# Kernel tuning notes

Measured on AMD Instinct MI355X. Metric: run time of the kernel, lower is better.

## Reference

```python
import jax, jax.numpy as jnp
import numpy as np
from jax.scipy.ndimage import map_coordinates

N = 512      # image H=W (x0.shape[2])
A = 30       # number of projection angles (sparse-view CT)
D = 729      # det_count (hardcoded in source)
L = 3        # LayerNo
B = 2        # batch
P = 2048     # FFT padding: next pow2 >= 2*D


def _ramp_filter(size):
    # standard Ram-Lak filter built in spatial domain (skimage/torch-radon style)
    n = np.concatenate((np.arange(1, size // 2 + 1, 2), np.arange(size // 2 - 1, 0, -2)))
    f = np.zeros(size)
    f[0] = 0.25
    f[1::2] = -1.0 / (np.pi * n) ** 2
    return jnp.asarray(2.0 * np.real(np.fft.fft(f))[: size // 2 + 1], dtype=jnp.float32)


def setup_inputs() -> dict:
    key = jax.random.key(0)
    ks = jax.random.split(key, 8)
    x0 = jax.random.normal(ks[0], (B, 1, N, N), jnp.float32)
    sinogram = jax.random.normal(ks[1], (B, 1, A, D), jnp.float32)
    theta = jnp.linspace(0.0, np.pi, A, endpoint=False).astype(jnp.float32)
    theta_label = theta
    # denoiser params, stacked over L unrolled layers
    w1 = jax.random.normal(ks[2], (L, 32, 1, 3, 3), jnp.float32) * 0.1
    b1 = jnp.zeros((L, 32), jnp.float32)
    w2 = jax.random.normal(ks[3], (L, 32, 32, 3, 3), jnp.float32) * 0.05
    b2 = jnp.zeros((L, 32), jnp.float32)
    w3 = jax.random.normal(ks[4], (L, 32, 32, 3, 3), jnp.float32) * 0.05
    b3 = jnp.zeros((L, 32), jnp.float32)
    w4 = jax.random.normal(ks[5], (L, 1, 32, 3, 3), jnp.float32) * 0.05
    steps = jnp.ones((L,), jnp.float32)  # step_n params (requires_grad=False)
    return {"cond": 1, "x0": x0, "sinogram": sinogram, "theta": theta,
            "theta_label": theta_label, "w1": w1, "b1": b1, "w2": w2, "b2": b2,
            "w3": w3, "b3": b3, "w4": w4, "steps": steps}


def _conv(x, w, b=None):
    y = jax.lax.conv_general_dilated(x, w, (1, 1), 'SAME',
                                     dimension_numbers=('NCHW', 'OIHW', 'NCHW'))
    return y if b is None else y + b[None, :, None, None]


def _denoiser(x, w1, b1, w2, b2, w3, b3, w4):
    h = jax.nn.relu(_conv(x, w1, b1))
    h = jax.nn.relu(_conv(h, w2, b2))
    h = jax.nn.relu(_conv(h, w3, b3))
    return _conv(h, w4)


def _geometry(theta):
    # parallel-beam ray sampling grid: rows/cols [A, D, T] with T=D samples (dt=1)
    c = (N - 1) / 2.0
    s = jnp.arange(D, dtype=jnp.float32) - (D - 1) / 2.0  # detector coords
    t = s                                                  # along-ray samples
    cs, sn = jnp.cos(theta), jnp.sin(theta)
    x = s[None, :, None] * cs[:, None, None] - t[None, None, :] * sn[:, None, None]
    y = s[None, :, None] * sn[:, None, None] + t[None, None, :] * cs[:, None, None]
    return y + c, x + c  # rows, cols


def _radon_fwd(imgs, rows, cols):
    # imgs [B,N,N] -> sinogram [B,A,D] via bilinear line-integral sampling
    sample = lambda im: map_coordinates(im, [rows, cols], order=1, mode='constant', cval=0.0)
    return jax.vmap(sample)(imgs).sum(-1)


def _filter_sino(sino, filt):
    F = jnp.fft.rfft(sino, n=P, axis=-1)
    g = jnp.fft.irfft(F * filt, n=P, axis=-1)[..., :D]
    return g * (jnp.pi / (2.0 * A))  # FBP normalization


def _backproj(sino, theta):
    # sino [B,A,D] -> image [B,N,N], linear interp along detector axis
    c = (N - 1) / 2.0
    xs = jnp.arange(N, dtype=jnp.float32) - c
    cs, sn = jnp.cos(theta), jnp.sin(theta)
    sgrid = cs[:, None, None] * xs[None, None, :] + sn[:, None, None] * xs[None, :, None]  # [A,N,N]
    idx = sgrid + (D - 1) / 2.0
    lo = jnp.floor(idx).astype(jnp.int32)
    w = idx - lo
    lo_ok = (lo >= 0) & (lo < D)
    hi_ok = (lo + 1 >= 0) & (lo + 1 < D)
    lo_c = jnp.clip(lo, 0, D - 1)
    hi_c = jnp.clip(lo + 1, 0, D - 1)
    a = jnp.arange(A)[:, None, None]
    v = sino[:, a, lo_c] * jnp.where(lo_ok, 1.0 - w, 0.0) + \
        sino[:, a, hi_c] * jnp.where(hi_ok, w, 0.0)       # [B,A,N,N]
    return v.sum(axis=1)


def reference(cond, x0, sinogram, theta, theta_label, w1, b1, w2, b2, w3, b3, w4, steps):
    rows, cols = _geometry(theta)
    filt = _ramp_filter(P)
    X = x0[:, 0]           # [B,N,N]
    sino = sinogram[:, 0]  # [B,A,D]
    for n in range(L):
        sino_pred = _radon_fwd(X, rows, cols)
        filtered = _filter_sino(sino_pred, filt)
        outputs = _backproj(sino - filtered, theta)
        z = X + steps[n] * outputs
        noise = _denoiser(X[:, None], w1[n], b1[n], w2[n], b2[n], w3[n], b3[n], w4[n])[:, 0]
        filtered_noise = _filter_sino(_radon_fwd(noise, rows, cols), filt)
        outputs_noise = _backproj(filtered_noise, theta)
        X = z + noise - steps[n] * outputs_noise
    Xo = X[:, None]
    return (Xo, Xo, Xo)
```

## Files before the change

kernel.cpp:

```cpp
#include <hip/hip_runtime.h>
#include <hip/hip_bf16.h>

typedef __hip_bfloat16 bf16;
typedef __attribute__((ext_vector_type(8))) short short8;
typedef __attribute__((ext_vector_type(4))) short s4v;
typedef __attribute__((ext_vector_type(4))) float float4v;

#define NN 512
#define NA 30
#define ND 729
#define NB 2
#define NL 3
#define BNN (NB*NN*NN)
#define BAD (NB*NA*ND)

#define PW 520
#define PH 516
#define PIMG (PH*PW)
#define POFF (2*PW + 2)

#define O_CS  0
#define O_SN  32
#define O_ICS 64
#define O_ISN 96
#define O_XP  128
#define O_YP  (O_XP + 2*PIMG)
#define O_SP  (O_YP + 2*PIMG)
#define O_Q   (O_SP + BAD)
#define O_WR  (O_Q + BAD)
#define O_H   (((O_WR + 34560) + 15) & ~15)
#define H_FLOATS (NB * 32 * NN * NN / 2)

#define WR2_OFF 0
#define WR3_OFF 27648
#define WR4_OFF 55296

__device__ __forceinline__ float2 ld2u(const float* p)
{
    float2 r;
    __builtin_memcpy(&r, p, 8);
    return r;
}

__global__ void k_prep(const float* __restrict__ theta,
                       const float* __restrict__ w2, const float* __restrict__ w3,
                       const float* __restrict__ w4, const float* __restrict__ x0,
                       float* __restrict__ ws, bf16* __restrict__ wr)
{
    int idx = blockIdx.x * 256 + threadIdx.x;
    if (idx < NA) {
        float t = theta[idx];
        float cs = cosf(t), sn = sinf(t);
        ws[O_CS + idx] = cs;
        ws[O_SN + idx] = sn;
        ws[O_ICS + idx] = 1.0f / cs;
        ws[O_ISN + idx] = -1.0f / sn;
    }
    if (idx < 2 * 27648) {
        const float* w = (idx < 27648) ? w2 : w3;
        int base = (idx < 27648) ? WR2_OFF : WR3_OFF;
        int r = idx % 27648;
        int n = r / 9216; int r2 = r % 9216;
        int tap = r2 / 1024; int r3 = r2 % 1024;
        int co = r3 / 32, ci = r3 % 32;
        wr[base + r] = __float2bfloat16(w[n * 9216 + (co * 32 + ci) * 9 + tap]);
    } else if (idx < 2 * 27648 + 3 * 4608) {
        int r = idx - 2 * 27648;
        int n = r / 4608; int r2 = r % 4608;
        int tap = r2 / 512; int r3 = r2 % 512;
        int co = r3 / 32, ci = r3 % 32;
        float v = (co == 0) ? w4[n * 288 + ci * 9 + tap] : 0.f;
        wr[WR4_OFF + r] = __float2bfloat16(v);
    }
    if (idx < 2 * PIMG) {
        int b = idx / PIMG, p = idx % PIMG;
        int y = p / PW, x = p % PW;
        bool interior = (y >= 2 && y < 2 + NN && x >= 2 && x < 2 + NN);
        float v = interior ? x0[b * NN * NN + (y - 2) * NN + (x - 2)] : 0.f;
        ws[O_XP + idx] = v;
        if (!interior) ws[O_YP + idx] = 0.f;
    }
}

__device__ __forceinline__ void isect2(float A, float inv, float lo, float hi,
                                       float& tlo, float& thi)
{
    float a = (lo - A) * inv, b = (hi - A) * inv;
    tlo = fmaxf(tlo, fminf(a, b));
    thi = fminf(thi, fmaxf(a, b));
}

__global__ __launch_bounds__(256) void k_radon(const float* __restrict__ img,
    const float* __restrict__ ws, float* __restrict__ out)
{
    int b = blockIdx.z, a = blockIdx.y;
    int wave = threadIdx.x >> 6;
    int lane = threadIdx.x & 63;
    int s = blockIdx.x * 4 + wave;
    if (s >= ND) return;
    float cs = ws[O_CS + a], sn = ws[O_SN + a];
    float ics = ws[O_ICS + a], isn = ws[O_ISN + a];
    float s_c = (float)s - 364.0f;
    float A_r = 255.5f + s_c * sn;
    float A_c = 255.5f + s_c * cs;

    float tlo = -1e9f, thi = 1e9f;
    isect2(A_r, ics, -1.0f, 512.0f, tlo, thi);
    isect2(A_c, isn, -1.0f, 512.0f, tlo, thi);
    float t0f = fmaxf(tlo + 364.0f, 0.0f);
    float t1f = fminf(thi + 364.0f, 728.0f);

    float acc = 0.f;
    if (t0f <= t1f) {
        int tb = (int)ceilf(t0f);
        int te = (int)floorf(t1f);
        const float* im = img + b * PIMG;
#pragma unroll 2
        for (int t = tb + lane; t <= te; t += 64) {
            float tc = (float)t - 364.0f;
            float r = fmaf(tc, cs, A_r);
            float c = fmaf(-tc, sn, A_c);
            float rf = floorf(r), cf = floorf(c);
            float dr = r - rf, dc = c - cf;
            int idx = (int)rf * PW + (int)cf;
            float2 tp = ld2u(im + idx);
            float2 bt = ld2u(im + idx + PW);
            float top = fmaf(dc, tp.y - tp.x, tp.x);
            float bot = fmaf(dc, bt.y - bt.x, bt.x);
            acc = fmaf(dr, bot - top, acc + top);
        }
    }
    acc += __shfl_down(acc, 32, 64);
    acc += __shfl_down(acc, 16, 64);
    acc += __shfl_down(acc, 8, 64);
    acc += __shfl_down(acc, 4, 64);
    acc += __shfl_down(acc, 2, 64);
    acc += __shfl_down(acc, 1, 64);
    if (lane == 0) out[(b * NA + a) * ND + s] = acc;
}

__global__ void k_filter(const float* __restrict__ sp, const float* __restrict__ sino,
                         float* __restrict__ q)
{
    __shared__ float row[ND];
    __shared__ float taps[364];
    int ba = blockIdx.y;
    const float* src = sp + ba * ND;
    for (int i = threadIdx.x; i < ND; i += 256) row[i] = src[i];
    const float PI2 = 9.86960440108936f;
    for (int i = threadIdx.x; i < 364; i += 256) {
        float m = (float)(2 * i + 1);
        taps[i] = -2.0f / (PI2 * m * m);
    }
    __syncthreads();
    const float scale = 0.0523598775598299f;
    int d = blockIdx.x * 256 + threadIdx.x;
    if (d < ND) {
        float g0 = 0.5f * row[d], g1 = 0.f;
#pragma unroll 4
        for (int j = 0; j < 364; j += 2) {
            int m0 = 2 * j + 1, m1 = 2 * j + 3;
            float l0 = (d - m0 >= 0) ? row[d - m0] : 0.f;
            float r0 = (d + m0 < ND) ? row[d + m0] : 0.f;
            g0 = fmaf(taps[j], l0 + r0, g0);
            float l1 = (d - m1 >= 0) ? row[d - m1] : 0.f;
            float r1 = (d + m1 < ND) ? row[d + m1] : 0.f;
            g1 = fmaf(taps[j + 1], l1 + r1, g1);
        }
        q[ba * ND + d] = sino[ba * ND + d] - scale * (g0 + g1);
    }
}

__global__ __launch_bounds__(256) void k_backproj_update(const float* __restrict__ q,
    const float* __restrict__ src1, const float* __restrict__ ws,
    const float* __restrict__ steps, int n, float* __restrict__ out,
    float* __restrict__ outcopy)
{
    __shared__ float qt[NA][28];
    __shared__ int dmin_s[NA];
    int b = blockIdx.z;
    int x0 = blockIdx.x * 16, y0 = blockIdx.y * 16;
    int tid = threadIdx.x;
    int lx = tid & 15, ly = tid >> 4;
    const float* qb = q + b * NA * ND;

    for (int idx = tid; idx < NA * 26; idx += 256) {
        int a = idx / 26, j = idx % 26;
        float cs = ws[O_CS + a], sn = ws[O_SN + a];
        float f00 = fmaf(cs, (float)x0 - 255.5f, fmaf(sn, (float)y0 - 255.5f, 364.0f));
        float fmn = f00 + fminf(cs * 15.f, 0.f) + fminf(sn * 15.f, 0.f);
        int dm = (int)floorf(fmn);
        if (j == 0) dmin_s[a] = dm;
        int d = dm + j;
        qt[a][j] = (d >= 0 && d < ND) ? qb[a * ND + d] : 0.f;
    }
    __syncthreads();

    float xc = (float)(x0 + lx) - 255.5f, yc = (float)(y0 + ly) - 255.5f;
    float acc = 0.f;
#pragma unroll
    for (int a = 0; a < NA; a++) {
        float cs = ws[O_CS + a], sn = ws[O_SN + a];
        float f = fmaf(cs, xc, fmaf(sn, yc, 364.0f));
        float lf = floorf(f);
        float w = f - lf;
        int j = (int)lf - dmin_s[a];
        float v0 = qt[a][j], v1 = qt[a][j + 1];
        acc = fmaf(v0, 1.0f - w, fmaf(v1, w, acc));
    }
    int pidx = b * PIMG + (y0 + ly) * PW + (x0 + lx);
    float v = fmaf(steps[n], acc, src1[pidx]);
    out[pidx] = v;
    if (outcopy) {
        int fidx = b * NN * NN + (y0 + ly) * NN + (x0 + lx);
        outcopy[fidx] = v;
        outcopy[fidx + BNN] = v;
        outcopy[fidx + 2 * BNN] = v;
    }
}

__global__ __launch_bounds__(256) void k_conv12(const float* __restrict__ XPb,
    const float* __restrict__ W1, const float* __restrict__ B1,
    const bf16* __restrict__ Wr2, const float* __restrict__ B2,
    bf16* __restrict__ outb)
{
    __shared__ bf16 h1t[34][18][32];
    int b = blockIdx.z;
    int x0 = blockIdx.x * 16;
    int Y0 = blockIdx.y * 32;
    const float* in = XPb + b * PIMG;

    for (int p = threadIdx.x; p < 34 * 18; p += 256) {
        int yy = p / 18, xx = p % 18;
        int gy = Y0 + yy - 1, gx = x0 + xx - 1;
        if (gy < 0 || gy >= NN || gx < 0 || gx >= NN) {
#pragma unroll
            for (int g = 0; g < 4; g++)
                *(short8*)(&h1t[yy][xx][g * 8]) = short8{};
        } else {
            float v[9];
#pragma unroll
            for (int dy = 0; dy < 3; dy++)
#pragma unroll
                for (int dx = 0; dx < 3; dx++)
                    v[dy * 3 + dx] = in[(gy + dy - 1) * PW + (gx + dx - 1)];
#pragma unroll
            for (int g = 0; g < 4; g++) {
                short8 pk;
#pragma unroll
                for (int j = 0; j < 8; j++) {
                    int co = g * 8 + j;
                    float a = B1[co];
                    const float* w = W1 + co * 9;
#pragma unroll
                    for (int k = 0; k < 9; k++) a = fmaf(v[k], w[k], a);
                    a = fmaxf(a, 0.f);
                    bf16 h = __float2bfloat16(a);
                    pk[j] = *reinterpret_cast<short*>(&h);
                }
                *(short8*)(&h1t[yy][xx][g * 8]) = pk;
            }
        }
    }
    __syncthreads();

    int lane = threadIdx.x & 63;
    int wave = threadIdx.x >> 6;
    int n16 = lane & 15, quad = lane >> 4;
    int y0w = Y0 + wave * 8;

    short8 wf[18];
#pragma unroll
    for (int tap = 0; tap < 9; tap++)
#pragma unroll
        for (int t = 0; t < 2; t++)
            wf[tap * 2 + t] = *(const short8*)(Wr2 + ((tap * 2 + t) * 16 + n16) * 32 + quad * 8);

    short8 win[3][3];
    auto loadrow = [&](int yy, short8* dst) {
        int ly = yy - (Y0 - 1);
#pragma unroll
        for (int dx = 0; dx < 3; dx++)
            dst[dx] = *(const short8*)(&h1t[ly][n16 + dx][quad * 8]);
    };
    loadrow(y0w - 1, win[0]);
    loadrow(y0w,     win[1]);

    float4v bias[2];
#pragma unroll
    for (int t = 0; t < 2; t++)
        bias[t] = *(const float4v*)(B2 + t * 16 + quad * 4);

    bf16* out = outb + (size_t)b * NN * NN * 32;
#pragma unroll
    for (int i = 0; i < 8; i++) {
        int y = y0w + i;
        loadrow(y + 1, win[(i + 2) % 3]);
        float4v acc[2];
#pragma unroll
        for (int t = 0; t < 2; t++) acc[t] = bias[t];
#pragma unroll
        for (int dy = 0; dy < 3; dy++) {
            short8* row = win[(i + dy) % 3];
#pragma unroll
            for (int dx = 0; dx < 3; dx++) {
                int tap = dy * 3 + dx;
#pragma unroll
                for (int t = 0; t < 2; t++)
                    acc[t] = __builtin_amdgcn_mfma_f32_16x16x32_bf16(wf[tap * 2 + t], row[dx], acc[t], 0, 0, 0);
            }
        }
        bf16* pp = out + ((size_t)y * NN + x0 + n16) * 32 + quad * 4;
#pragma unroll
        for (int t = 0; t < 2; t++) {
            s4v pk;
#pragma unroll
            for (int r = 0; r < 4; r++) {
                float v = fmaxf(acc[t][r], 0.f);
                bf16 h = __float2bfloat16(v);
                pk[r] = *reinterpret_cast<short*>(&h);
            }
            *(s4v*)(pp + t * 16) = pk;
        }
    }
}

#define SH 8
template<int NCO, bool RELU, bool HASB, bool OUTF32>
__global__ __launch_bounds__(256) void k_conv_stream(const bf16* __restrict__ inb,
    const bf16* __restrict__ Wr, const float* __restrict__ Bs,
    const float* __restrict__ addsrc, void* __restrict__ outv)
{
    int lane = threadIdx.x & 63;
    int wave = threadIdx.x >> 6;
    int n16 = lane & 15, quad = lane >> 4;
    int b = blockIdx.z;
    int x0 = blockIdx.x * 16;
    int y0 = (blockIdx.y * 4 + wave) * SH;
    const bf16* in = inb + (size_t)b * NN * NN * 32;

    short8 wf[9 * NCO];
#pragma unroll
    for (int tap = 0; tap < 9; tap++)
#pragma unroll
        for (int t = 0; t < NCO; t++)
            wf[tap * NCO + t] = *(const short8*)(Wr + ((tap * NCO + t) * 16 + n16) * 32 + quad * 8);

    bool vx[3];
#pragma unroll
    for (int dx = 0; dx < 3; dx++) {
        int xx = x0 + n16 + dx - 1;
        vx[dx] = (xx >= 0) && (xx < NN);
    }

    short8 win[3][3];
    auto loadrow = [&](int yy, short8* dst) {
        if (yy >= 0 && yy < NN) {
            const bf16* rowp = in + (size_t)yy * NN * 32;
#pragma unroll
            for (int dx = 0; dx < 3; dx++) {
                short8 v = {};
                if (vx[dx]) v = *(const short8*)(rowp + (x0 + n16 + dx - 1) * 32 + quad * 8);
                dst[dx] = v;
            }
        } else {
            dst[0] = short8{}; dst[1] = short8{}; dst[2] = short8{};
        }
    };
    loadrow(y0 - 1, win[0]);
    loadrow(y0,     win[1]);

    float4v bias[NCO];
#pragma unroll
    for (int t = 0; t < NCO; t++)
        bias[t] = HASB ? *(const float4v*)(Bs + t * 16 + quad * 4) : (float4v){0.f, 0.f, 0.f, 0.f};

#pragma unroll
    for (int i = 0; i < SH; i++) {
        int y = y0 + i;
        loadrow(y + 1, win[(i + 2) % 3]);
        float4v acc[NCO];
#pragma unroll
        for (int t = 0; t < NCO; t++) acc[t] = bias[t];
#pragma unroll
        for (int dy = 0; dy < 3; dy++) {
            short8* row = win[(i + dy) % 3];
#pragma unroll
            for (int dx = 0; dx < 3; dx++) {
                int tap = dy * 3 + dx;
#pragma unroll
                for (int t = 0; t < NCO; t++)
                    acc[t] = __builtin_amdgcn_mfma_f32_16x16x32_bf16(wf[tap * NCO + t], row[dx], acc[t], 0, 0, 0);
            }
        }
        if (OUTF32) {
            float* out = (float*)outv + b * PIMG;
            if (quad == 0) {
                int pi = y * PW + x0 + n16;
                out[pi] = addsrc[b * PIMG + pi] + acc[0][0];
            }
        } else {
            bf16* out = (bf16*)outv + (size_t)b * NN * NN * 32;
            bf16* pp = out + ((size_t)y * NN + x0 + n16) * 32 + quad * 4;
#pragma unroll
            for (int t = 0; t < NCO; t++) {
                s4v pk;
#pragma unroll
                for (int r = 0; r < 4; r++) {
                    float v = acc[t][r];
                    if (RELU) v = fmaxf(v, 0.f);
                    bf16 h = __float2bfloat16(v);
                    pk[r] = *reinterpret_cast<short*>(&h);
                }
                *(s4v*)(pp + t * 16) = pk;
            }
        }
    }
}

extern "C" void kernel_launch(void* const* d_in, const int* in_sizes, int n_in,
                              void* d_out, int out_size, void* d_ws, size_t ws_size,
                              hipStream_t stream)
{
    const float* x0    = (const float*)d_in[1];
    const float* sg    = (const float*)d_in[2];
    const float* theta = (const float*)d_in[3];
    const float* w1    = (const float*)d_in[5];
    const float* b1    = (const float*)d_in[6];
    const float* w2    = (const float*)d_in[7];
    const float* b2    = (const float*)d_in[8];
    const float* w3    = (const float*)d_in[9];
    const float* b3    = (const float*)d_in[10];
    const float* w4    = (const float*)d_in[11];
    const float* steps = (const float*)d_in[12];

    float* ws = (float*)d_ws;
    float* XP = ws + O_XP + POFF;
    float* YP = ws + O_YP + POFF;
    float* SP = ws + O_SP;
    float* Q  = ws + O_Q;
    bf16* wr  = (bf16*)(ws + O_WR);
    bf16* h1  = (bf16*)(ws + O_H);
    bf16* h2  = (bf16*)(ws + O_H + H_FLOATS);

    k_prep<<<(2 * PIMG + 255) / 256, 256, 0, stream>>>(theta, w2, w3, w4, x0, ws, wr);

    for (int n = 0; n < NL; n++) {
        k_conv12<<<dim3(32, 16, NB), 256, 0, stream>>>(
            XP, w1 + n * 288, b1 + n * 32, wr + WR2_OFF + n * 9216, b2 + n * 32, h2);
        k_conv_stream<2, true, true, false><<<dim3(32, 16, NB), 256, 0, stream>>>(
            h2, wr + WR3_OFF + n * 9216, b3 + n * 32, nullptr, h1);
        k_conv_stream<1, false, false, true><<<dim3(32, 16, NB), 256, 0, stream>>>(
            h1, wr + WR4_OFF + n * 4608, nullptr, XP, YP);

        k_radon<<<dim3((ND + 3) / 4, NA, NB), 256, 0, stream>>>(YP, ws, SP);
        k_filter<<<dim3(3, NB * NA), 256, 0, stream>>>(SP, sg, Q);
        k_backproj_update<<<dim3(32, 32, NB), 256, 0, stream>>>(
            Q, YP, ws, steps, n, XP, (n == NL - 1) ? (float*)d_out : nullptr);
    }
}
```

Measured before the change: 431.8 us.

## Fuse conv3 and conv4 through an LDS halo tile

Replaces the two separate streaming conv kernels (conv3 with ReLU into a bf16 32-channel buffer, then conv4 into the float image) with one kernel. Each block computes a 34x18 halo tile of conv3 output into shared memory and then runs conv4 from LDS. This removes the global write and re-read of the 32-channel h1 intermediate (about 32 MB per layer) and one launch per layer. In exchange it recomputes halo rows and columns: two 16-wide strips are computed to cover 18 columns, roughly double the conv3 MFMA work, and it uses about 39 KB of LDS per block, which may limit occupancy.

```diff
diff --git a/kernel.cpp b/kernel.cpp
--- a/kernel.cpp
+++ b/kernel.cpp
@@ -325,94 +325,133 @@
     }
 }
 
-#define SH 8
-template<int NCO, bool RELU, bool HASB, bool OUTF32>
-__global__ __launch_bounds__(256) void k_conv_stream(const bf16* __restrict__ inb,
-    const bf16* __restrict__ Wr, const float* __restrict__ Bs,
-    const float* __restrict__ addsrc, void* __restrict__ outv)
-{
+__global__ __launch_bounds__(256) void k_conv34(const bf16* __restrict__ h2b,
+    const bf16* __restrict__ Wr3, const float* __restrict__ B3,
+    const bf16* __restrict__ Wr4, const float* __restrict__ XPb,
+    float* __restrict__ YPb)
+{
+    __shared__ bf16 h1t[34][18][32];
+    int b = blockIdx.z;
+    int x0 = blockIdx.x * 16;
+    int Y0 = blockIdx.y * 32;
+    const bf16* in = h2b + (size_t)b * NN * NN * 32;
+
     int lane = threadIdx.x & 63;
     int wave = threadIdx.x >> 6;
     int n16 = lane & 15, quad = lane >> 4;
-    int b = blockIdx.z;
-    int x0 = blockIdx.x * 16;
-    int y0 = (blockIdx.y * 4 + wave) * SH;
-    const bf16* in = inb + (size_t)b * NN * NN * 32;
-
-    short8 wf[9 * NCO];
-#pragma unroll
-    for (int tap = 0; tap < 9; tap++)
-#pragma unroll
-        for (int t = 0; t < NCO; t++)
-            wf[tap * NCO + t] = *(const short8*)(Wr + ((tap * NCO + t) * 16 + n16) * 32 + quad * 8);
-
-    bool vx[3];
-#pragma unroll
-    for (int dx = 0; dx < 3; dx++) {
-        int xx = x0 + n16 + dx - 1;
-        vx[dx] = (xx >= 0) && (xx < NN);
-    }
-
-    short8 win[3][3];
-    auto loadrow = [&](int yy, short8* dst) {
-        if (yy >= 0 && yy < NN) {
-            const bf16* rowp = in + (size_t)yy * NN * 32;
-#pragma unroll
-            for (int dx = 0; dx < 3; dx++) {
-                short8 v = {};
-                if (vx[dx]) v = *(const short8*)(rowp + (x0 + n16 + dx - 1) * 32 + quad * 8);
-                dst[dx] = v;
-            }
-        } else {
-            dst[0] = short8{}; dst[1] = short8{}; dst[2] = short8{};
-        }
-    };
-    loadrow(y0 - 1, win[0]);
-    loadrow(y0,     win[1]);
-
-    float4v bias[NCO];
-#pragma unroll
-    for (int t = 0; t < NCO; t++)
-        bias[t] = HASB ? *(const float4v*)(Bs + t * 16 + quad * 4) : (float4v){0.f, 0.f, 0.f, 0.f};
-
-#pragma unroll
-    for (int i = 0; i < SH; i++) {
-        int y = y0 + i;
-        loadrow(y + 1, win[(i + 2) % 3]);
-        float4v acc[NCO];
-#pragma unroll
-        for (int t = 0; t < NCO; t++) acc[t] = bias[t];
-#pragma unroll
-        for (int dy = 0; dy < 3; dy++) {
-            short8* row = win[(i + dy) % 3];
-#pragma unroll
-            for (int dx = 0; dx < 3; dx++) {
-                int tap = dy * 3 + dx;
-#pragma unroll
-                for (int t = 0; t < NCO; t++)
-                    acc[t] = __builtin_amdgcn_mfma_f32_16x16x32_bf16(wf[tap * NCO + t], row[dx], acc[t], 0, 0, 0);
-            }
-        }
-        if (OUTF32) {
-            float* out = (float*)outv + b * PIMG;
+
+    {
+        int strip = wave & 1, half = wave >> 1;
+        int sx = x0 - 1 + strip * 2;
+        int ly0 = half * 17;
+        int gy0 = Y0 - 1 + ly0;
+
+        short8 wf[18];
+#pragma unroll
+        for (int tap = 0; tap < 9; tap++)
+#pragma unroll
+            for (int t = 0; t < 2; t++)
+                wf[tap * 2 + t] = *(const short8*)(Wr3 + ((tap * 2 + t) * 16 + n16) * 32 + quad * 8);
+
+        bool vx[3];
+#pragma unroll
+        for (int dx = 0; dx < 3; dx++) {
+            int xx = sx + n16 + dx - 1;
+            vx[dx] = (xx >= 0) && (xx < NN);
+        }
+        short8 win[3][3];
+        auto loadrow = [&](int yy, short8* dst) {
+            if (yy >= 0 && yy < NN) {
+                const bf16* rowp = in + (size_t)yy * NN * 32;
+#pragma unroll
+                for (int dx = 0; dx < 3; dx++) {
+                    short8 v = {};
+                    if (vx[dx]) v = *(const short8*)(rowp + (sx + n16 + dx - 1) * 32 + quad * 8);
+                    dst[dx] = v;
+                }
+            } else {
+                dst[0] = short8{}; dst[1] = short8{}; dst[2] = short8{};
+            }
+        };
+        loadrow(gy0 - 1, win[0]);
+        loadrow(gy0,     win[1]);
+
+        float4v bias[2];
+#pragma unroll
+        for (int t = 0; t < 2; t++)
+            bias[t] = *(const float4v*)(B3 + t * 16 + quad * 4);
+
+        bool wr = (strip == 0) || (n16 >= 14);
+        int px = n16 + strip * 2;
+        for (int i = 0; i < 17; i++) {
+            int y = gy0 + i;
+            loadrow(y + 1, win[(i + 2) % 3]);
+            float4v acc[2];
+#pragma unroll
+            for (int t = 0; t < 2; t++) acc[t] = bias[t];
+#pragma unroll
+            for (int dy = 0; dy < 3; dy++) {
+                short8* row = win[(i + dy) % 3];
+#pragma unroll
+                for (int dx = 0; dx < 3; dx++) {
+                    int tap = dy * 3 + dx;
+#pragma unroll
+                    for (int t = 0; t < 2; t++)
+                        acc[t] = __builtin_amdgcn_mfma_f32_16x16x32_bf16(wf[tap * 2 + t], row[dx], acc[t], 0, 0, 0);
+                }
+            }
+            if (wr) {
+                int ly = ly0 + i;
+#pragma unroll
+                for (int t = 0; t < 2; t++) {
+                    s4v pk;
+#pragma unroll
+                    for (int r = 0; r < 4; r++) {
+                        float v = fmaxf(acc[t][r], 0.f);
+                        bf16 h = __float2bfloat16(v);
+                        pk[r] = *reinterpret_cast<short*>(&h);
+                    }
+                    *(s4v*)(&h1t[ly][px][t * 16 + quad * 4]) = pk;
+                }
+            }
+        }
+    }
+    __syncthreads();
+
+    {
+        int y0w = Y0 + wave * 8;
+        short8 wf[9];
+#pragma unroll
+        for (int tap = 0; tap < 9; tap++)
+            wf[tap] = *(const short8*)(Wr4 + (tap * 16 + n16) * 32 + quad * 8);
+
+        short8 win[3][3];
+        auto ldsrow = [&](int yy, short8* dst) {
+            int ly = yy - (Y0 - 1);
+#pragma unroll
+            for (int dx = 0; dx < 3; dx++)
+                dst[dx] = *(const short8*)(&h1t[ly][n16 + dx][quad * 8]);
+        };
+        ldsrow(y0w - 1, win[0]);
+        ldsrow(y0w,     win[1]);
+
+        const float* xp = XPb + b * PIMG;
+        float* yp = YPb + b * PIMG;
+#pragma unroll
+        for (int i = 0; i < 8; i++) {
+            int y = y0w + i;
+            ldsrow(y + 1, win[(i + 2) % 3]);
+            float4v acc = {0.f, 0.f, 0.f, 0.f};
+#pragma unroll
+            for (int dy = 0; dy < 3; dy++) {
+                short8* row = win[(i + dy) % 3];
+#pragma unroll
+                for (int dx = 0; dx < 3; dx++)
+                    acc = __builtin_amdgcn_mfma_f32_16x16x32_bf16(wf[dy * 3 + dx], row[dx], acc, 0, 0, 0);
+            }
             if (quad == 0) {
                 int pi = y * PW + x0 + n16;
-                out[pi] = addsrc[b * PIMG + pi] + acc[0][0];
-            }
-        } else {
-            bf16* out = (bf16*)outv + (size_t)b * NN * NN * 32;
-            bf16* pp = out + ((size_t)y * NN + x0 + n16) * 32 + quad * 4;
-#pragma unroll
-            for (int t = 0; t < NCO; t++) {
-                s4v pk;
-#pragma unroll
-                for (int r = 0; r < 4; r++) {
-                    float v = acc[t][r];
-                    if (RELU) v = fmaxf(v, 0.f);
-                    bf16 h = __float2bfloat16(v);
-                    pk[r] = *reinterpret_cast<short*>(&h);
-                }
-                *(s4v*)(pp + t * 16) = pk;
+                yp[pi] = xp[pi] + acc[0];
             }
         }
     }
@@ -440,18 +479,15 @@
     float* SP = ws + O_SP;
     float* Q  = ws + O_Q;
     bf16* wr  = (bf16*)(ws + O_WR);
-    bf16* h1  = (bf16*)(ws + O_H);
-    bf16* h2  = (bf16*)(ws + O_H + H_FLOATS);
+    bf16* h2  = (bf16*)(ws + O_H);
 
     k_prep<<<(2 * PIMG + 255) / 256, 256, 0, stream>>>(theta, w2, w3, w4, x0, ws, wr);
 
     for (int n = 0; n < NL; n++) {
         k_conv12<<<dim3(32, 16, NB), 256, 0, stream>>>(
             XP, w1 + n * 288, b1 + n * 32, wr + WR2_OFF + n * 9216, b2 + n * 32, h2);
-        k_conv_stream<2, true, true, false><<<dim3(32, 16, NB), 256, 0, stream>>>(
-            h2, wr + WR3_OFF + n * 9216, b3 + n * 32, nullptr, h1);
-        k_conv_stream<1, false, false, true><<<dim3(32, 16, NB), 256, 0, stream>>>(
-            h1, wr + WR4_OFF + n * 4608, nullptr, XP, YP);
+        k_conv34<<<dim3(32, 16, NB), 256, 0, stream>>>(
+            h2, wr + WR3_OFF + n * 9216, b3 + n * 32, wr + WR4_OFF + n * 4608, XP, YP);
 
         k_radon<<<dim3((ND + 3) / 4, NA, NB), 256, 0, stream>>>(YP, ws, SP);
         k_filter<<<dim3(3, NB * NA), 256, 0, stream>>>(SP, sg, Q);
```

New measurement: 438.3 us. About the same (+1.5%).

## Add transposed image copy so radon samples along contiguous rows for steep angles

Applied to the files above, without the earlier changes.

The final conv kernel now also writes a transposed copy of the padded image into a new workspace buffer. For angles where |cos| >= |sin|, the radon kernel samples from that copy, so consecutive lanes step mostly along contiguous memory instead of across rows. This targets uncoalesced gathers in the forward projection. The cost is an extra strided (uncoalesced) scattered write per pixel in the conv epilogue and one more image-sized buffer.

```diff
diff --git a/kernel.cpp b/kernel.cpp
--- a/kernel.cpp
+++ b/kernel.cpp
@@ -25,7 +25,8 @@
 #define O_ISN 96
 #define O_XP  128
 #define O_YP  (O_XP + 2*PIMG)
-#define O_SP  (O_YP + 2*PIMG)
+#define O_YPT (O_YP + 2*PIMG)
+#define O_SP  (O_YPT + 2*PIMG)
 #define O_Q   (O_SP + BAD)
 #define O_WR  (O_Q + BAD)
 #define O_H   (((O_WR + 34560) + 15) & ~15)
@@ -78,7 +79,10 @@
         bool interior = (y >= 2 && y < 2 + NN && x >= 2 && x < 2 + NN);
         float v = interior ? x0[b * NN * NN + (y - 2) * NN + (x - 2)] : 0.f;
         ws[O_XP + idx] = v;
-        if (!interior) ws[O_YP + idx] = 0.f;
+        if (!interior) {
+            ws[O_YP + idx] = 0.f;
+            ws[O_YPT + idx] = 0.f;
+        }
     }
 }
 
@@ -91,7 +95,8 @@
 }
 
 __global__ __launch_bounds__(256) void k_radon(const float* __restrict__ img,
-    const float* __restrict__ ws, float* __restrict__ out)
+    const float* __restrict__ imgT, const float* __restrict__ ws,
+    float* __restrict__ out)
 {
     int b = blockIdx.z, a = blockIdx.y;
     int wave = threadIdx.x >> 6;
@@ -110,11 +115,13 @@
     float t0f = fmaxf(tlo + 364.0f, 0.0f);
     float t1f = fminf(thi + 364.0f, 728.0f);
 
+    bool useT = fabsf(cs) >= fabsf(sn);
+    const float* im = (useT ? imgT : img) + b * PIMG;
+
     float acc = 0.f;
     if (t0f <= t1f) {
         int tb = (int)ceilf(t0f);
         int te = (int)floorf(t1f);
-        const float* im = img + b * PIMG;
 #pragma unroll 2
         for (int t = tb + lane; t <= te; t += 64) {
             float tc = (float)t - 364.0f;
@@ -122,12 +129,15 @@
             float c = fmaf(-tc, sn, A_c);
             float rf = floorf(r), cf = floorf(c);
             float dr = r - rf, dc = c - cf;
-            int idx = (int)rf * PW + (int)cf;
-            float2 tp = ld2u(im + idx);
-            float2 bt = ld2u(im + idx + PW);
-            float top = fmaf(dc, tp.y - tp.x, tp.x);
-            float bot = fmaf(dc, bt.y - bt.x, bt.x);
-            acc = fmaf(dr, bot - top, acc + top);
+            int irr = (int)rf, icc = (int)cf;
+            int idx = useT ? (icc * PW + irr) : (irr * PW + icc);
+            float da = useT ? dr : dc;
+            float db = useT ? dc : dr;
+            float2 p1 = ld2u(im + idx);
+            float2 p2 = ld2u(im + idx + PW);
+            float u = fmaf(da, p1.y - p1.x, p1.x);
+            float w = fmaf(da, p2.y - p2.x, p2.x);
+            acc = fmaf(db, w - u, acc + u);
         }
     }
     acc += __shfl_down(acc, 32, 64);
@@ -329,7 +339,8 @@
 template<int NCO, bool RELU, bool HASB, bool OUTF32>
 __global__ __launch_bounds__(256) void k_conv_stream(const bf16* __restrict__ inb,
     const bf16* __restrict__ Wr, const float* __restrict__ Bs,
-    const float* __restrict__ addsrc, void* __restrict__ outv)
+    const float* __restrict__ addsrc, void* __restrict__ outv,
+    float* __restrict__ outT)
 {
     int lane = threadIdx.x & 63;
     int wave = threadIdx.x >> 6;
@@ -396,8 +407,10 @@
         if (OUTF32) {
             float* out = (float*)outv + b * PIMG;
             if (quad == 0) {
-                int pi = y * PW + x0 + n16;
-                out[pi] = addsrc[b * PIMG + pi] + acc[0][0];
+                int px = x0 + n16;
+                float vv = addsrc[b * PIMG + y * PW + px] + acc[0][0];
+                out[y * PW + px] = vv;
+                outT[b * PIMG + px * PW + y] = vv;
             }
         } else {
             bf16* out = (bf16*)outv + (size_t)b * NN * NN * 32;
@@ -435,8 +448,9 @@
     const float* steps = (const float*)d_in[12];
 
     float* ws = (float*)d_ws;
-    float* XP = ws + O_XP + POFF;
-    float* YP = ws + O_YP + POFF;
+    float* XP  = ws + O_XP + POFF;
+    float* YP  = ws + O_YP + POFF;
+    float* YPT = ws + O_YPT + POFF;
     float* SP = ws + O_SP;
     float* Q  = ws + O_Q;
     bf16* wr  = (bf16*)(ws + O_WR);
@@ -449,11 +463,11 @@
         k_conv12<<<dim3(32, 16, NB), 256, 0, stream>>>(
             XP, w1 + n * 288, b1 + n * 32, wr + WR2_OFF + n * 9216, b2 + n * 32, h2);
         k_conv_stream<2, true, true, false><<<dim3(32, 16, NB), 256, 0, stream>>>(
-            h2, wr + WR3_OFF + n * 9216, b3 + n * 32, nullptr, h1);
+            h2, wr + WR3_OFF + n * 9216, b3 + n * 32, nullptr, h1, nullptr);
         k_conv_stream<1, false, false, true><<<dim3(32, 16, NB), 256, 0, stream>>>(
-            h1, wr + WR4_OFF + n * 4608, nullptr, XP, YP);
-
-        k_radon<<<dim3((ND + 3) / 4, NA, NB), 256, 0, stream>>>(YP, ws, SP);
+            h1, wr + WR4_OFF + n * 4608, nullptr, XP, YP, YPT);
+
+        k_radon<<<dim3((ND + 3) / 4, NA, NB), 256, 0, stream>>>(YP, YPT, ws, SP);
         k_filter<<<dim3(3, NB * NA), 256, 0, stream>>>(SP, sg, Q);
         k_backproj_update<<<dim3(32, 32, NB), 256, 0, stream>>>(
             Q, YP, ws, steps, n, XP, (n == NL - 1) ? (float*)d_out : nullptr);
```

Measured after the change: 417.8 us. 1.03x faster.
